# Performance work log

Measured on AMD Instinct MI355X. Metric: run time of the kernel, lower is better.

The kernel has to match this reference:

```python
import jax, jax.numpy as jnp
import numpy as np

UNITS = 14336
IN_FEATURES = 4096
PACKED = IN_FEATURES // 4  # 4 ternary values (2 bits each) per byte
CLIP_VAL = 100.0

# 2-bit crumb -> ternary value lookup: 0 -> 0, 1 -> +1, 2 -> -1, 3 -> 0
_TERNARY_LUT = jnp.array([0.0, 1.0, -1.0, 0.0], dtype=jnp.float32)


def _unpack_ternary(pw):
    """pw: [U, P] int (byte values 0..255) -> dense ternary float W [U, 4*P].
    Little-endian crumbs within each byte (shifts 0,2,4,6)."""
    crumbs = jnp.stack([(pw >> (2 * i)) & 3 for i in range(4)], axis=-1)  # [U, P, 4]
    crumbs = crumbs.reshape(pw.shape[0], -1)  # [U, 4*P]
    return _TERNARY_LUT[crumbs][:, :IN_FEATURES]  # [U, IN]


def setup_inputs() -> dict:
    key = jax.random.key(0)
    k1, k2, k3, k4 = jax.random.split(key, 4)
    x = jax.random.normal(k1, (32, IN_FEATURES), dtype=jnp.float32)
    # packed ternary weights, one uint8-valued byte per 4 ternary weights
    pw = jax.random.randint(k2, (UNITS, PACKED), 0, 256, dtype=jnp.int32)
    scale = 1.0 + 0.02 * jax.random.normal(k3, (UNITS,), dtype=jnp.float32)
    bias = 0.01 * jax.random.normal(k4, (UNITS,), dtype=jnp.float32)
    return {"x": x, "pw": pw, "scale": scale, "bias": bias}


def reference(x, pw, scale, bias):
    # dense ternary weight [UNITS, IN]; kernel target would fuse this unpack into the GEMM
    W = _unpack_ternary(pw)
    y = jnp.einsum('bd,ud->bu', x, W)  # [B, UNITS]
    y = y * scale + bias               # per-unit affine dequant
    return jnp.clip(y, -CLIP_VAL, CLIP_VAL)
```

## Files before the change

### kernel.cpp

```cpp
#include <hip/hip_runtime.h>

#define UNITS 14336
#define IN_F 4096
#define PACKED 1024
#define CLIP_VAL 100.0f

typedef unsigned int uint32;

using bf16x8 = __attribute__((ext_vector_type(8))) short;
using f32x4  = __attribute__((ext_vector_type(4))) float;

__device__ inline unsigned short f2bf(float f) {
    uint32 u = __float_as_uint(f);
    u += 0x7FFFu + ((u >> 16) & 1u);
    return (unsigned short)(u >> 16);
}

__device__ inline uint32 pack2bf(float a, float b) {
    return (uint32)f2bf(a) | ((uint32)f2bf(b) << 16);
}

__device__ inline void unpack_byte(int v, uint32& r0, uint32& r1) {
    uint32 t0 = ((uint32)v & 3u) | (((uint32)v & 0xCu) << 14);
    uint32 t1 = (((uint32)v >> 4) & 3u) | (((uint32)v & 0xC0u) << 10);
    uint32 s0 = t0 >> 1;
    uint32 s1 = t1 >> 1;
    uint32 nz0 = (t0 ^ s0) & 0x00010001u;
    uint32 nz1 = (t1 ^ s1) & 0x00010001u;
    r0 = nz0 * 0x3F80u + ((s0 & 0x00010001u) << 15);
    r1 = nz1 * 0x3F80u + ((s1 & 0x00010001u) << 15);
}

__device__ inline float clipf(float y) {
    return fminf(fmaxf(y, -CLIP_VAL), CLIP_VAL);
}


__global__ __launch_bounds__(256) void convert_x_kernel(
    const float* __restrict__ x, uint4* __restrict__ ws) {
    int t = blockIdx.x * 256 + threadIdx.x;
    int lane = t & 63;
    int h = (t >> 6) & 1;
    int s = (t >> 7) & 1;
    int g = t >> 8;
    int n = lane & 15;
    int q = lane >> 4;
    int b = h * 16 + n;
    int k0 = g * 64 + q * 16 + s * 8;
    const float4* src = (const float4*)(x + (size_t)b * IN_F + k0);
    float4 lo = src[0];
    float4 hi = src[1];
    uint4 o;
    o.x = pack2bf(lo.x, lo.y);
    o.y = pack2bf(lo.z, lo.w);
    o.z = pack2bf(hi.x, hi.y);
    o.w = pack2bf(hi.z, hi.w);
    ws[t] = o;
}

__global__ __launch_bounds__(512) void ternary_mm_kernel(
    const uint4* __restrict__ xw,
    const int*   __restrict__ pw,
    const float* __restrict__ scale,
    const float* __restrict__ bias,
    float*       __restrict__ out) {
    __shared__ f32x4 red[8][2][64];

    const int tid  = threadIdx.x;
    const int wid  = tid >> 6;
    const int lane = tid & 63;
    const int q    = lane >> 4;
    const int n    = lane & 15;
    const int u0   = blockIdx.x << 4;

    f32x4 acc0 = {0.f,0.f,0.f,0.f};
    f32x4 acc1 = {0.f,0.f,0.f,0.f};

    const int g0 = wid << 3;
    const int*   pA = pw + (size_t)(u0 + n) * PACKED + (g0 << 4) + (q << 2);
    const uint4* xb = xw + (g0 << 8) + lane;

    #pragma unroll 4
    for (int i = 0; i < 8; ++i) {
        int4 w4 = *(const int4*)(pA + (i << 4));
        uint4 x00 = xb[(i << 8)];
        uint4 x01 = xb[(i << 8) + 64];
        uint4 x10 = xb[(i << 8) + 128];
        uint4 x11 = xb[(i << 8) + 192];

        uint4 fA, fB;
        unpack_byte(w4.x, fA.x, fA.y);
        unpack_byte(w4.y, fA.z, fA.w);
        unpack_byte(w4.z, fB.x, fB.y);
        unpack_byte(w4.w, fB.z, fB.w);
        bf16x8 vA = __builtin_bit_cast(bf16x8, fA);
        bf16x8 vB = __builtin_bit_cast(bf16x8, fB);

        acc0 = __builtin_amdgcn_mfma_f32_16x16x32_bf16(
            __builtin_bit_cast(bf16x8, x00), vA, acc0, 0, 0, 0);
        acc1 = __builtin_amdgcn_mfma_f32_16x16x32_bf16(
            __builtin_bit_cast(bf16x8, x01), vA, acc1, 0, 0, 0);
        acc0 = __builtin_amdgcn_mfma_f32_16x16x32_bf16(
            __builtin_bit_cast(bf16x8, x10), vB, acc0, 0, 0, 0);
        acc1 = __builtin_amdgcn_mfma_f32_16x16x32_bf16(
            __builtin_bit_cast(bf16x8, x11), vB, acc1, 0, 0, 0);
    }

    red[wid][0][lane] = acc0;
    red[wid][1][lane] = acc1;
    __syncthreads();

    if (tid < 128) {
        const int h = tid >> 6;
        const int l = tid & 63;
        f32x4 s = red[0][h][l];
        #pragma unroll
        for (int w = 1; w < 8; ++w) {
            f32x4 v = red[w][h][l];
            s[0] += v[0]; s[1] += v[1]; s[2] += v[2]; s[3] += v[3];
        }
        const int u  = u0 + (l & 15);
        const int b0 = h * 16 + ((l >> 4) << 2);
        const float sc = scale[u];
        const float bi = bias[u];
        float* o = out + (size_t)b0 * UNITS + u;
        o[0 * UNITS] = clipf(s[0] * sc + bi);
        o[1 * UNITS] = clipf(s[1] * sc + bi);
        o[2 * UNITS] = clipf(s[2] * sc + bi);
        o[3 * UNITS] = clipf(s[3] * sc + bi);
    }
}

extern "C" void kernel_launch(void* const* d_in, const int* in_sizes, int n_in,
                              void* d_out, int out_size, void* d_ws, size_t ws_size,
                              hipStream_t stream) {
    const float* x     = (const float*)d_in[0];
    const int*   pw    = (const int*)d_in[1];
    const float* scale = (const float*)d_in[2];
    const float* bias  = (const float*)d_in[3];
    float* out = (float*)d_out;

    uint4* xw = (uint4*)d_ws;

    convert_x_kernel<<<64, 256, 0, stream>>>(x, xw);
    ternary_mm_kernel<<<UNITS / 16, 512, 0, stream>>>(xw, pw, scale, bias, out);
}
```

Before: 109.7 us.

## Stage packed weights through LDS with coalesced loads, compacting int32 to bytes

Each block first loads its 16 rows of int32-packed weights with coalesced 16-byte global loads, compacts four int32 values into one 32-bit word of bytes, and writes them to a padded shared-memory buffer. The MFMA loop then reads a single uint32 per iteration from LDS instead of a strided int4 global load per lane. The loop is fully unrolled and launch bounds request higher occupancy. This is meant to improve global access coalescing for the dominant weight stream, at the cost of about 16KB of extra LDS per block and a preload phase that does not overlap with compute.

```diff
diff --git a/kernel.cpp b/kernel.cpp
--- a/kernel.cpp
+++ b/kernel.cpp
@@ -20,9 +20,9 @@
     return (uint32)f2bf(a) | ((uint32)f2bf(b) << 16);
 }
 
-__device__ inline void unpack_byte(int v, uint32& r0, uint32& r1) {
-    uint32 t0 = ((uint32)v & 3u) | (((uint32)v & 0xCu) << 14);
-    uint32 t1 = (((uint32)v >> 4) & 3u) | (((uint32)v & 0xC0u) << 10);
+__device__ inline void unpack_byte(uint32 v, uint32& r0, uint32& r1) {
+    uint32 t0 = (v & 3u) | ((v & 0xCu) << 14);
+    uint32 t1 = ((v >> 4) & 3u) | ((v & 0xC0u) << 10);
     uint32 s0 = t0 >> 1;
     uint32 s1 = t1 >> 1;
     uint32 nz0 = (t0 ^ s0) & 0x00010001u;
@@ -58,12 +58,13 @@
     ws[t] = o;
 }
 
-__global__ __launch_bounds__(512) void ternary_mm_kernel(
+__global__ __launch_bounds__(512, 8) void ternary_mm_kernel(
     const uint4* __restrict__ xw,
     const int*   __restrict__ pw,
     const float* __restrict__ scale,
     const float* __restrict__ bias,
     float*       __restrict__ out) {
+    __shared__ char  stg[16 * 1040];
     __shared__ f32x4 red[8][2][64];
 
     const int tid  = threadIdx.x;
@@ -72,27 +73,43 @@
     const int q    = lane >> 4;
     const int n    = lane & 15;
     const int u0   = blockIdx.x << 4;
+    const int g0   = wid << 3;
+
+    {
+        const char* src = (const char*)pw;
+        #pragma unroll
+        for (int j = 0; j < 8; ++j) {
+            const int j2 = j >> 1;
+            const int hh = j & 1;
+            const int row = (j2 << 2) + q;
+            const int cc  = (wid << 5) + (hh << 4) + n;
+            uint4 v = *(const uint4*)(src + (size_t)(u0 + row) * 4096
+                                          + ((size_t)cc << 4));
+            uint32 d = (v.x & 0xFFu) | ((v.y & 0xFFu) << 8)
+                     | ((v.z & 0xFFu) << 16) | ((v.w & 0xFFu) << 24);
+            *(uint32*)(stg + row * 1040 + (cc << 2)) = d;
+        }
+    }
+
+    const uint4* xb = xw + (g0 << 8) + lane;
+    const char*  lb = stg + n * 1040 + (((wid << 5) + q) << 2);
 
     f32x4 acc0 = {0.f,0.f,0.f,0.f};
     f32x4 acc1 = {0.f,0.f,0.f,0.f};
 
-    const int g0 = wid << 3;
-    const int*   pA = pw + (size_t)(u0 + n) * PACKED + (g0 << 4) + (q << 2);
-    const uint4* xb = xw + (g0 << 8) + lane;
-
-    #pragma unroll 4
+    #pragma unroll
     for (int i = 0; i < 8; ++i) {
-        int4 w4 = *(const int4*)(pA + (i << 4));
         uint4 x00 = xb[(i << 8)];
         uint4 x01 = xb[(i << 8) + 64];
         uint4 x10 = xb[(i << 8) + 128];
         uint4 x11 = xb[(i << 8) + 192];
+        uint32 w = *(const uint32*)(lb + (i << 4));
 
         uint4 fA, fB;
-        unpack_byte(w4.x, fA.x, fA.y);
-        unpack_byte(w4.y, fA.z, fA.w);
-        unpack_byte(w4.z, fB.x, fB.y);
-        unpack_byte(w4.w, fB.z, fB.w);
+        unpack_byte(w & 0xFFu,         fA.x, fA.y);
+        unpack_byte((w >> 8) & 0xFFu,  fA.z, fA.w);
+        unpack_byte((w >> 16) & 0xFFu, fB.x, fB.y);
+        unpack_byte(w >> 24,           fB.z, fB.w);
         bf16x8 vA = __builtin_bit_cast(bf16x8, fA);
         bf16x8 vB = __builtin_bit_cast(bf16x8, fB);
 
```

Result: faster. 104.1 us (-5.1%).
